# Performance work log

Hardware: AMD Instinct MI355X
Metric: run time of the kernel (lower is better)

The kernel has to match this reference:

```python
import jax, jax.numpy as jnp
import numpy as np

# irreps layout: in/out = 32x0e + 8x1o  (dim 32 + 24 = 56), sh = 1x0e + 1x1o (dim 4)
NS, NV = 32, 8
N_NODES, N_EDGES, N_EDGE_FEAT, HIDDEN = 10000, 100000, 64, 64
W_NUMEL = NS*NS + NS*NV + NV*NV + NV*NS  # 1600
EPS = 1e-5
# path normalization (e3nn-style 'component'/'element'):
# fan_in into 0e output = 32 (0x0 path) + 8 (1x1 path) = 40; same for 1o output.
INV40 = 1.0 / np.sqrt(40.0)            # paths with trivial/identity CG net factor
INV120 = 1.0 / np.sqrt(120.0)          # paths with w3j = delta/sqrt(3) extra factor


def setup_inputs() -> dict:
    key = jax.random.key(0)
    ks = jax.random.split(key, 12)
    node_attr = jax.random.normal(ks[0], (N_NODES, 56), dtype=jnp.float32)
    edge_attr = jax.random.normal(ks[1], (N_EDGES, N_EDGE_FEAT), dtype=jnp.float32)
    edge_sh = jax.random.normal(ks[2], (N_EDGES, 4), dtype=jnp.float32)
    edge_index = jax.random.randint(ks[3], (2, N_EDGES), 0, N_NODES, dtype=jnp.int64)
    s1 = 1.0 / np.sqrt(N_EDGE_FEAT)
    s2 = 1.0 / np.sqrt(HIDDEN)
    fc1_w = jax.random.normal(ks[4], (N_EDGE_FEAT, HIDDEN), dtype=jnp.float32) * s1
    fc1_b = jnp.zeros((HIDDEN,), dtype=jnp.float32)
    fc2_w = jax.random.normal(ks[5], (HIDDEN, W_NUMEL), dtype=jnp.float32) * s2
    fc2_b = jnp.zeros((W_NUMEL,), dtype=jnp.float32)
    bn_gamma0 = jnp.ones((NS,), dtype=jnp.float32)
    bn_beta0 = jnp.zeros((NS,), dtype=jnp.float32)
    bn_gamma1 = jnp.ones((NV,), dtype=jnp.float32)
    return dict(node_attr=node_attr, edge_attr=edge_attr, edge_sh=edge_sh,
                edge_index=edge_index, fc1_w=fc1_w, fc1_b=fc1_b,
                fc2_w=fc2_w, fc2_b=fc2_b, bn_gamma0=bn_gamma0,
                bn_beta0=bn_beta0, bn_gamma1=bn_gamma1)


def _forward(node_attr, edge_attr, edge_sh, fc1_w, fc1_b, fc2_w, fc2_b,
             bn_gamma0, bn_beta0, bn_gamma1, edge_index):
    E = edge_attr.shape[0]
    N = node_attr.shape[0]
    edge_src, edge_dst = edge_index[0], edge_index[1]

    # edge MLP -> per-edge tensor-product weights [E, 1600]
    h = jax.nn.relu(edge_attr @ fc1_w + fc1_b)
    w = h @ fc2_w + fc2_b
    o1 = NS * NS            # 0e x 0e -> 0e
    o2 = o1 + NS * NV       # 0e x 1o -> 1o
    o3 = o2 + NV * NV       # 1o x 0e -> 1o
    w00 = w[:, :o1].reshape(E, NS, NS)
    w01 = w[:, o1:o2].reshape(E, NS, NV)
    w10 = w[:, o2:o3].reshape(E, NV, NV)
    w11 = w[:, o3:].reshape(E, NV, NS)

    # gather node features at destination, split into scalar / vector irreps
    x = node_attr[edge_dst]                  # [E, 56]
    x0 = x[:, :NS]                           # [E, 32] scalars
    x1 = x[:, NS:].reshape(E, NV, 3)         # [E, 8, 3] l=1 vectors
    s0 = edge_sh[:, 0]                       # [E]
    s1 = edge_sh[:, 1:4]                     # [E, 3]

    # Clebsch-Gordan paths (w3j(1,1,0)=w3j(1,0,1)=w3j(0,1,1)=delta/sqrt(3))
    out0 = jnp.einsum('eu,euw->ew', x0 * s0[:, None], w00) * INV40 \
         + jnp.einsum('eui,ei,euw->ew', x1, s1, w11) * INV120
    out1 = jnp.einsum('eu,ei,euw->ewi', x0, s1, w01) * INV40 \
         + jnp.einsum('eui,euw->ewi', x1 * s0[:, None, None], w10) * INV40
    tp_out = jnp.concatenate([out0, out1.reshape(E, NV * 3)], axis=-1)  # [E, 56]

    # scatter-mean over edge_src
    sums = jax.ops.segment_sum(tp_out, edge_src, num_segments=N)
    cnt = jax.ops.segment_sum(jnp.ones((E,), tp_out.dtype), edge_src, num_segments=N)
    out = sums / jnp.maximum(cnt, 1.0)[:, None]

    # residual (in_dim == out_dim, pad is a no-op)
    out = out + node_attr

    # e3nn-style BatchNorm (training statistics, reduce='mean')
    sc = out[:, :NS]
    vec = out[:, NS:].reshape(N, NV, 3)
    m = sc.mean(axis=0)
    sc_c = sc - m
    var = (sc_c ** 2).mean(axis=0)
    sc_n = sc_c * jax.lax.rsqrt(var + EPS) * bn_gamma0 + bn_beta0
    vnorm = (vec ** 2).mean(axis=-1).mean(axis=0)          # [NV]
    vec_n = vec * (jax.lax.rsqrt(vnorm + EPS) * bn_gamma1)[None, :, None]
    return jnp.concatenate([sc_n, vec_n.reshape(N, NV * 3)], axis=-1)


def reference(node_attr, edge_attr, edge_sh, edge_index, fc1_w, fc1_b,
              fc2_w, fc2_b, bn_gamma0, bn_beta0, bn_gamma1):
    return _forward(node_attr, edge_attr, edge_sh, fc1_w, fc1_b, fc2_w,
                    fc2_b, bn_gamma0, bn_beta0, bn_gamma1, edge_index)
```

## Files before the change

### kernel.cpp

```cpp
#include <hip/hip_runtime.h>

typedef __attribute__((ext_vector_type(4))) float f32x4;
typedef __attribute__((ext_vector_type(2))) float f32x2;
typedef __attribute__((ext_vector_type(8))) short bf16x8;

#define NEDGE 100000
#define NNODE 10000
#define INV40f 0.15811388300841897f
#define INV120f 0.09128709291752769f

__device__ inline short f2bf(float f) {
    unsigned u = __builtin_bit_cast(unsigned, f);
    u = (u + 0x7fffu + ((u >> 16) & 1u)) >> 16;
    return (short)u;
}

__device__ __forceinline__ float bperm(int byteIdx, float v) {
    return __builtin_bit_cast(float,
        __builtin_amdgcn_ds_bpermute(byteIdx, __builtin_bit_cast(int, v)));
}

__device__ __forceinline__ void stage16(const void* gsrc, void* ldst) {
    __builtin_amdgcn_global_load_lds(
        (const __attribute__((address_space(1))) unsigned*)gsrc,
        (__attribute__((address_space(3))) unsigned*)(unsigned long long)(uintptr_t)ldst,
        16, 0, 0);
}

#define MFMA16(A,B,C) __builtin_amdgcn_mfma_f32_16x16x32_bf16((A),(B),(C),0,0,0)

__global__ __launch_bounds__(256) void prep(const float* __restrict__ fc1_w,
                                            const float* __restrict__ fc2_w,
                                            short* __restrict__ fc1_wt,
                                            short* __restrict__ fc2_wt,
                                            float* __restrict__ stats,
                                            int* __restrict__ hist) {
    const int b = blockIdx.x, t = threadIdx.x;
    if (b < 25) {
        __shared__ short tile[64 * 66];
        const int c0 = b * 64;
        #pragma unroll
        for (int rep = 0; rep < 16; rep++) {
            const int idx = rep * 256 + t;
            const int k = idx >> 6, c = idx & 63;
            tile[k * 66 + c] = f2bf(fc2_w[(size_t)k * 1600 + c0 + c]);
        }
        __syncthreads();
        #pragma unroll
        for (int rep = 0; rep < 16; rep++) {
            const int idx = rep * 256 + t;
            const int c = idx >> 6, k = idx & 63;
            fc2_wt[(size_t)(c0 + c) * 64 + k] = tile[k * 66 + c];
        }
    } else if (b == 25) {
        #pragma unroll
        for (int rep = 0; rep < 16; rep++) {
            const int i = rep * 256 + t;
            fc1_wt[(i & 63) * 64 + (i >> 6)] = f2bf(fc1_w[i]);
        }
    } else if (b == 26) {
        if (t < 72) stats[t] = 0.0f;
    } else {
        const int i = (b - 27) * 256 + t;
        if (i < NNODE) hist[i] = 0;
    }
}

__global__ __launch_bounds__(512, 4) void edge_fused(
    const float* __restrict__ node_attr,
    const float* __restrict__ edge_attr,
    const float* __restrict__ edge_sh,
    const int*   __restrict__ edge_index,
    const float* __restrict__ fc1_b,
    const float* __restrict__ fc2_b,
    const short* __restrict__ fc1_wt,
    const short* __restrict__ fc2_wt,
    float* __restrict__ tp_out,
    int*   __restrict__ hist)
{
    __shared__ __align__(16) char lds[51200];
    char* cbA = lds;
    char* cbB = lds + 16384;

    const int tid  = threadIdx.x;
    const int wid  = tid >> 6;
    const int wtid = tid & 63;
    const int l15  = wtid & 15;
    const int lg   = wtid >> 4;
    const int lg4  = lg * 4;
    const int e0   = blockIdx.x * 128 + wid * 16;
    const bool active = (e0 < NEDGE);

    char*  h_s = lds + 32768 + wid * 2048;
    float* shb = (float*)(lds + 49152 + wid * 256);

#define STAGE1(CH, BUF, J) do { \
        const int _o = (wid * 2 + (J)) * 1024 + wtid * 16; \
        const int _g = _o ^ (((_o >> 7) & 7) << 4); \
        stage16((const char*)fc2_wt + (CH) * 16384 + _g, (BUF) + (wid * 2 + (J)) * 1024); \
    } while (0)
#define STAGE_FULL(CH, BUF) do { STAGE1(CH, BUF, 0); STAGE1(CH, BUF, 1); } while (0)
#define STAGE_TAIL(CH, BUF) do { if (wid < 4) { STAGE1(CH, BUF, 0); STAGE1(CH, BUF, 1); } } while (0)

    STAGE_FULL(0, cbA);

    int dst_r = 0;
    if (active && wtid < 16) {
        dst_r = edge_index[NEDGE + e0 + wtid];
        const int src = edge_index[e0 + wtid];
        const f32x4 sh_r = *(const f32x4*)(edge_sh + (size_t)(e0 + wtid) * 4);
        atomicAdd(&hist[src], 1);
        *(f32x4*)(shb + wtid * 4) = sh_r;
    }

    bf16x8 ha0, ha1;
    f32x4 shv = {0.f, 0.f, 0.f, 0.f};
    float c00r[8], cb1r[8], c10r[6], c11r[2];
    int vidx[4];
    #pragma unroll
    for (int g = 0; g < 4; g++) vidx[g] = (g * 16 + l15) * 4;

    if (active) {
        const float* pa = edge_attr + (size_t)(e0 + l15) * 64 + lg * 8;
        const f32x4 va0 = *(const f32x4*)(pa);
        const f32x4 va1 = *(const f32x4*)(pa + 4);
        const f32x4 va2 = *(const f32x4*)(pa + 32);
        const f32x4 va3 = *(const f32x4*)(pa + 36);

        const int dstm = __shfl(dst_r, l15, 64);
        const float* nap = node_attr + (size_t)dstm * 56;
        const f32x4 x0a = *(const f32x4*)(nap + lg * 8);
        const f32x4 x0b = *(const f32x4*)(nap + lg * 8 + 4);
        const f32x2 x1a = *(const f32x2*)(nap + 32 + lg * 6);
        const f32x2 x1b = *(const f32x2*)(nap + 34 + lg * 6);
        const f32x2 x1c = *(const f32x2*)(nap + 36 + lg * 6);
        shv = *(const f32x4*)(shb + l15 * 4);

        const float s0 = shv[0];
        #pragma unroll
        for (int j = 0; j < 4; j++) {
            cb1r[j]     = INV40f * x0a[j];
            cb1r[4 + j] = INV40f * x0b[j];
            c00r[j]     = s0 * cb1r[j];
            c00r[4 + j] = s0 * cb1r[4 + j];
        }
        const float i40s0 = INV40f * s0;
        c10r[0] = i40s0 * x1a[0]; c10r[1] = i40s0 * x1a[1]; c10r[2] = i40s0 * x1b[0];
        c10r[3] = i40s0 * x1b[1]; c10r[4] = i40s0 * x1c[0]; c10r[5] = i40s0 * x1c[1];
        c11r[0] = INV120f * (x1a[0]*shv[1] + x1a[1]*shv[2] + x1b[0]*shv[3]);
        c11r[1] = INV120f * (x1b[1]*shv[1] + x1c[0]*shv[2] + x1c[1]*shv[3]);

        bf16x8 a0, a1;
        #pragma unroll
        for (int i = 0; i < 4; i++) {
            a0[i] = f2bf(va0[i]); a0[4+i] = f2bf(va1[i]);
            a1[i] = f2bf(va2[i]); a1[4+i] = f2bf(va3[i]);
        }
        #pragma unroll
        for (int nf0 = 0; nf0 < 4; nf0++) {
            const bf16x8 b0 = *(const bf16x8*)(fc1_wt + (nf0*16 + l15)*64 + lg*8);
            const bf16x8 b1 = *(const bf16x8*)(fc1_wt + (nf0*16 + l15)*64 + 32 + lg*8);
            const float bias = fc1_b[nf0*16 + l15];
            f32x4 c = {bias, bias, bias, bias};
            c = MFMA16(a0, b0, c);
            c = MFMA16(a1, b1, c);
            #pragma unroll
            for (int reg = 0; reg < 4; reg++) {
                const int row = lg4 + reg;
                *(short*)(h_s + ((row*128 + (nf0*16 + l15)*2) ^ ((row & 7) << 4))) =
                    f2bf(fmaxf(c[reg], 0.0f));
            }
        }
        ha0 = *(const bf16x8*)(h_s + ((l15*128 +      lg*16) ^ ((l15 & 7) << 4)));
        ha1 = *(const bf16x8*)(h_s + ((l15*128 + 64 + lg*16) ^ ((l15 & 7) << 4)));
    }

    const int s_swz = (l15 & 7) << 4;
    const int ro0 = (l15 * 128 + lg * 16) ^ s_swz;
    const int ro1 = (l15 * 128 + lg * 16 + 64) ^ s_swz;
    const int usel = lg >> 1;
    float acc0[2][4] = {{0,0,0,0},{0,0,0,0}};
    float ab1[4] = {0,0,0,0};
    float b2v[12] = {};

    auto frag = [&](const char* cb, int nfl, int nf) -> f32x4 {
        const bf16x8 b0 = *(const bf16x8*)(cb + nfl * 2048 + ro0);
        const bf16x8 b1 = *(const bf16x8*)(cb + nfl * 2048 + ro1);
        f32x4 c = *(const f32x4*)(fc2_b + nf * 16 + lg4);
        c = MFMA16(b0, ha0, c);
        return MFMA16(b1, ha1, c);
    };
    auto cons_w00 = [&](const char* cb, int ch) {
        #pragma unroll
        for (int nfl = 0; nfl < 8; nfl++) {
            const int nf = ch * 8 + nfl;
            const f32x4 c = frag(cb, nfl, nf);
            const int u = nf >> 1, hi = nf & 1;
            const float cv = bperm(vidx[u >> 3], c00r[u & 7]);
            #pragma unroll
            for (int reg = 0; reg < 4; reg++) acc0[hi][reg] += cv * c[reg];
        }
    };
    auto cons_w01 = [&](const char* cb, int rbase) {
        #pragma unroll
        for (int i = 0; i < 8; i++) {
            const int nfl_r = rbase + i;
            const f32x4 c = frag(cb, i, 64 + nfl_r);
            const int r0 = (2 * nfl_r) & 7, g = nfl_r >> 2;
            const float e0v = bperm(vidx[g], cb1r[r0]);
            const float e1v = bperm(vidx[g], cb1r[r0 + 1]);
            const float cv = usel ? e1v : e0v;
            #pragma unroll
            for (int reg = 0; reg < 4; reg++) ab1[reg] += cv * c[reg];
        }
    };
    auto cons_w10 = [&](const char* cb, int fb) {
        #pragma unroll
        for (int nfl = 0; nfl < 4; nfl++) {
            const f32x4 c = frag(cb, fb + nfl, 80 + nfl);
            #pragma unroll
            for (int i = 0; i < 3; i++) {
                const float e0v = bperm(vidx[nfl], c10r[i]);
                const float e1v = bperm(vidx[nfl], c10r[3 + i]);
                const float cv = usel ? e1v : e0v;
                #pragma unroll
                for (int reg = 0; reg < 4; reg++) b2v[reg * 3 + i] += cv * c[reg];
            }
        }
    };
    auto cons_w11 = [&](const char* cb, int fb, int ridx0, int cnt) {
        #pragma unroll
        for (int i = 0; i < 8; i++) {
            if (i >= cnt) break;
            const int ridx = ridx0 + i;
            const f32x4 c = frag(cb, fb + i, 84 + ridx);
            const int up = ridx >> 1, hi = ridx & 1;
            const float cv = bperm(vidx[up >> 1], c11r[up & 1]);
            #pragma unroll
            for (int reg = 0; reg < 4; reg++) acc0[hi][reg] += cv * c[reg];
        }
    };

    __syncthreads();
    STAGE_FULL(1,  cbB); if (active) cons_w00(cbA, 0); __syncthreads();
    STAGE_FULL(2,  cbA); if (active) cons_w00(cbB, 1); __syncthreads();
    STAGE_FULL(3,  cbB); if (active) cons_w00(cbA, 2); __syncthreads();
    STAGE_FULL(4,  cbA); if (active) cons_w00(cbB, 3); __syncthreads();
    STAGE_FULL(5,  cbB); if (active) cons_w00(cbA, 4); __syncthreads();
    STAGE_FULL(6,  cbA); if (active) cons_w00(cbB, 5); __syncthreads();
    STAGE_FULL(7,  cbB); if (active) cons_w00(cbA, 6); __syncthreads();
    STAGE_FULL(8,  cbA); if (active) cons_w00(cbB, 7); __syncthreads();
    STAGE_FULL(9,  cbB); if (active) cons_w01(cbA, 0); __syncthreads();
    STAGE_FULL(10, cbA); if (active) cons_w01(cbB, 8); __syncthreads();
    STAGE_FULL(11, cbB); if (active) { cons_w10(cbA, 0); cons_w11(cbA, 4, 0, 4); } __syncthreads();
    STAGE_TAIL(12, cbA); if (active) cons_w11(cbB, 0, 4, 8);   __syncthreads();
                         if (active) cons_w11(cbA, 0, 12, 4);

    if (!active) return;

    float* orow = tp_out + (size_t)(e0 + l15) * 56;
    {
        const f32x4 o0 = {acc0[0][0], acc0[0][1], acc0[0][2], acc0[0][3]};
        const f32x4 o1 = {acc0[1][0], acc0[1][1], acc0[1][2], acc0[1][3]};
        *(f32x4*)(orow + lg4)      = o0;
        *(f32x4*)(orow + 16 + lg4) = o1;
    }
    #pragma unroll
    for (int reg = 0; reg < 4; reg++) ab1[reg] += __shfl_xor(ab1[reg], 32, 64);
    #pragma unroll
    for (int m = 0; m < 12; m++) b2v[m] += __shfl_xor(b2v[m], 32, 64);
    if (lg < 2) {
        float ov[12];
        #pragma unroll
        for (int reg = 0; reg < 4; reg++) {
            ov[reg*3 + 0] = shv[1] * ab1[reg] + b2v[reg*3 + 0];
            ov[reg*3 + 1] = shv[2] * ab1[reg] + b2v[reg*3 + 1];
            ov[reg*3 + 2] = shv[3] * ab1[reg] + b2v[reg*3 + 2];
        }
        float* p1 = orow + 32 + lg * 12;
        *(f32x4*)(p1)     = f32x4{ov[0], ov[1], ov[2],  ov[3]};
        *(f32x4*)(p1 + 4) = f32x4{ov[4], ov[5], ov[6],  ov[7]};
        *(f32x4*)(p1 + 8) = f32x4{ov[8], ov[9], ov[10], ov[11]};
    }
#undef STAGE1
#undef STAGE_FULL
#undef STAGE_TAIL
}

__global__ __launch_bounds__(1024) void scan_hist(const int* __restrict__ hist,
                                                  int* __restrict__ offsets,
                                                  int* __restrict__ cursor) {
    __shared__ int part[1024];
    const int t = threadIdx.x;
    const int n0 = t * 10;
    int lh[10];
    int s = 0;
    if (n0 < NNODE) {
        #pragma unroll
        for (int j = 0; j < 10; j++) { lh[j] = hist[n0 + j]; s += lh[j]; }
    }
    part[t] = s;
    __syncthreads();
    for (int d = 1; d < 1024; d <<= 1) {
        const int v = (t >= d) ? part[t - d] : 0;
        __syncthreads();
        part[t] += v;
        __syncthreads();
    }
    if (n0 < NNODE) {
        int run = part[t] - s;
        #pragma unroll
        for (int j = 0; j < 10; j++) {
            offsets[n0 + j] = run; cursor[n0 + j] = run; run += lh[j];
        }
    }
    if (t == 0) offsets[NNODE] = NEDGE;
}

__global__ __launch_bounds__(256) void fill_perm(const int* __restrict__ edge_index,
                                                 int* __restrict__ cursor,
                                                 int* __restrict__ perm) {
    const int e = blockIdx.x * 256 + threadIdx.x;
    if (e < NEDGE) {
        const int s = edge_index[e];
        const int p = atomicAdd(&cursor[s], 1);
        perm[p] = e;
    }
}

__global__ __launch_bounds__(256) void node_agg(
    const float* __restrict__ tp_out, const int* __restrict__ offsets,
    const int* __restrict__ perm,
    const float* __restrict__ node_attr, float* __restrict__ out,
    float* __restrict__ stats)
{
    __shared__ float part[72];
    const int tid = threadIdx.x;
    if (tid < 72) part[tid] = 0.0f;
    __syncthreads();
    const int n = blockIdx.x * 16 + (tid >> 4);
    const int q = tid & 15;
    if (n < NNODE && q < 14) {
        const int st = offsets[n], en = offsets[n + 1];
        f32x4 acc = {0.f, 0.f, 0.f, 0.f};
        for (int r = st; r < en; r++)
            acc += *(const f32x4*)(tp_out + (size_t)perm[r] * 56 + q * 4);
        const float inv = 1.0f / fmaxf((float)(en - st), 1.0f);
        const int c0 = q * 4;
        const f32x4 res = *(const f32x4*)(node_attr + (size_t)n * 56 + c0);
        f32x4 val;
        #pragma unroll
        for (int j = 0; j < 4; j++) {
            val[j] = acc[j] * inv + res[j];
            const int c = c0 + j;
            if (c < 32) {
                atomicAdd(&part[c], val[j]);
                atomicAdd(&part[32 + c], val[j] * val[j]);
            } else {
                atomicAdd(&part[64 + (c - 32) / 3], val[j] * val[j]);
            }
        }
        *(f32x4*)(out + (size_t)n * 56 + c0) = val;
    }
    __syncthreads();
    if (tid < 72) unsafeAtomicAdd(&stats[tid], part[tid]);
}

__global__ __launch_bounds__(256) void node_norm(
    float* __restrict__ out, const float* __restrict__ stats,
    const float* __restrict__ g0, const float* __restrict__ b0,
    const float* __restrict__ g1)
{
    const int id = blockIdx.x * 256 + threadIdx.x;
    if (id >= NNODE * 56) return;
    const int c = id % 56;
    float val = out[id];
    if (c < 32) {
        const float m   = stats[c]      * (1.0f / NNODE);
        const float ex2 = stats[32 + c] * (1.0f / NNODE);
        const float var = ex2 - m * m;
        val = (val - m) * rsqrtf(var + 1e-5f) * g0[c] + b0[c];
    } else {
        const int v = (c - 32) / 3;
        const float vn = stats[64 + v] * (1.0f / (3.0f * NNODE));
        val = val * rsqrtf(vn + 1e-5f) * g1[v];
    }
    out[id] = val;
}

extern "C" void kernel_launch(void* const* d_in, const int* in_sizes, int n_in,
                              void* d_out, int out_size, void* d_ws, size_t ws_size,
                              hipStream_t stream) {
    const float* node_attr = (const float*)d_in[0];
    const float* edge_attr = (const float*)d_in[1];
    const float* edge_sh   = (const float*)d_in[2];
    const int*   edge_index= (const int*)  d_in[3];
    const float* fc1_w     = (const float*)d_in[4];
    const float* fc1_b     = (const float*)d_in[5];
    const float* fc2_w     = (const float*)d_in[6];
    const float* fc2_b     = (const float*)d_in[7];
    const float* g0        = (const float*)d_in[8];
    const float* b0        = (const float*)d_in[9];
    const float* g1        = (const float*)d_in[10];
    float* out = (float*)d_out;

    char* ws = (char*)d_ws;
    float* stats   = (float*)(ws + 0);
    int*   hist    = (int*)  (ws + 288);
    int*   offsets = (int*)  (ws + 40288);
    int*   cursor  = (int*)  (ws + 80320);
    int*   perm    = (int*)  (ws + 120320);
    short* fc1_wt  = (short*)(ws + 520320);
    short* fc2_wt  = (short*)(ws + 528512);
    float* tp_out  = (float*)(ws + 733312);

    prep<<<67, 256, 0, stream>>>(fc1_w, fc2_w, fc1_wt, fc2_wt, stats, hist);
    edge_fused<<<782, 512, 0, stream>>>(node_attr, edge_attr, edge_sh, edge_index,
                                        fc1_b, fc2_b, fc1_wt, fc2_wt, tp_out, hist);
    scan_hist<<<1, 1024, 0, stream>>>(hist, offsets, cursor);
    fill_perm<<<391, 256, 0, stream>>>(edge_index, cursor, perm);
    node_agg<<<625, 256, 0, stream>>>(tp_out, offsets, perm, node_attr, out, stats);
    node_norm<<<2188, 256, 0, stream>>>(out, stats, g0, b0, g1);
}
```

Measured before the change: 110.8 us.

## Prefetch fc2 fragments in registers, stage bias in LDS, use wave-shuffle scan

The fc2 consumer loops now keep a rolling 2-3 deep software pipeline of LDS B-fragment loads and bias loads in registers, so LDS latency overlaps the MFMAs. The fc2 bias is staged once per block into shared memory instead of being read from global memory for every fragment. The single-block histogram scan is rewritten as a 256-thread wave-shuffle scan with 40 nodes per thread, replacing the 1024-thread LDS scan and its many barriers. The tail stage now loads a full chunk. This raises LDS use and register pressure, which could lower occupancy.

```diff
diff --git a/kernel.cpp b/kernel.cpp
--- a/kernel.cpp
+++ b/kernel.cpp
@@ -78,9 +78,10 @@
     float* __restrict__ tp_out,
     int*   __restrict__ hist)
 {
-    __shared__ __align__(16) char lds[51200];
+    __shared__ __align__(16) char lds[57600];
     char* cbA = lds;
     char* cbB = lds + 16384;
+    float* bias_s = (float*)(lds + 51200);
 
     const int tid  = threadIdx.x;
     const int wid  = tid >> 6;
@@ -100,9 +101,12 @@
         stage16((const char*)fc2_wt + (CH) * 16384 + _g, (BUF) + (wid * 2 + (J)) * 1024); \
     } while (0)
 #define STAGE_FULL(CH, BUF) do { STAGE1(CH, BUF, 0); STAGE1(CH, BUF, 1); } while (0)
-#define STAGE_TAIL(CH, BUF) do { if (wid < 4) { STAGE1(CH, BUF, 0); STAGE1(CH, BUF, 1); } } while (0)
 
     STAGE_FULL(0, cbA);
+
+    if (tid < 400) {
+        *(f32x4*)(bias_s + tid * 4) = *(const f32x4*)(fc2_b + tid * 4);
+    }
 
     int dst_r = 0;
     if (active && wtid < 16) {
@@ -175,26 +179,35 @@
         ha1 = *(const bf16x8*)(h_s + ((l15*128 + 64 + lg*16) ^ ((l15 & 7) << 4)));
     }
 
-    const int s_swz = (l15 & 7) << 4;
-    const int ro0 = (l15 * 128 + lg * 16) ^ s_swz;
-    const int ro1 = (l15 * 128 + lg * 16 + 64) ^ s_swz;
+    const int hswz = (l15 & 7) << 4;
+    const int ro0 = (l15 * 128 + lg * 16) ^ hswz;
+    const int ro1 = (l15 * 128 + lg * 16 + 64) ^ hswz;
     const int usel = lg >> 1;
     float acc0[2][4] = {{0,0,0,0},{0,0,0,0}};
     float ab1[4] = {0,0,0,0};
     float b2v[12] = {};
 
-    auto frag = [&](const char* cb, int nfl, int nf) -> f32x4 {
-        const bf16x8 b0 = *(const bf16x8*)(cb + nfl * 2048 + ro0);
-        const bf16x8 b1 = *(const bf16x8*)(cb + nfl * 2048 + ro1);
-        f32x4 c = *(const f32x4*)(fc2_b + nf * 16 + lg4);
-        c = MFMA16(b0, ha0, c);
-        return MFMA16(b1, ha1, c);
-    };
     auto cons_w00 = [&](const char* cb, int ch) {
-        #pragma unroll
-        for (int nfl = 0; nfl < 8; nfl++) {
-            const int nf = ch * 8 + nfl;
-            const f32x4 c = frag(cb, nfl, nf);
+        bf16x8 pb0[3], pb1[3]; f32x4 pc[3];
+        #pragma unroll
+        for (int k = 0; k < 3; k++) {
+            pb0[k] = *(const bf16x8*)(cb + k * 2048 + ro0);
+            pb1[k] = *(const bf16x8*)(cb + k * 2048 + ro1);
+            pc[k]  = *(const f32x4*)(bias_s + (ch * 8 + k) * 16 + lg4);
+        }
+        #pragma unroll
+        for (int i = 0; i < 8; i++) {
+            const int s = i % 3;
+            const bf16x8 b0 = pb0[s], b1 = pb1[s];
+            f32x4 c = pc[s];
+            if (i + 3 < 8) {
+                pb0[s] = *(const bf16x8*)(cb + (i + 3) * 2048 + ro0);
+                pb1[s] = *(const bf16x8*)(cb + (i + 3) * 2048 + ro1);
+                pc[s]  = *(const f32x4*)(bias_s + (ch * 8 + i + 3) * 16 + lg4);
+            }
+            c = MFMA16(b0, ha0, c);
+            c = MFMA16(b1, ha1, c);
+            const int nf = ch * 8 + i;
             const int u = nf >> 1, hi = nf & 1;
             const float cv = bperm(vidx[u >> 3], c00r[u & 7]);
             #pragma unroll
@@ -202,10 +215,26 @@
         }
     };
     auto cons_w01 = [&](const char* cb, int rbase) {
+        bf16x8 pb0[3], pb1[3]; f32x4 pc[3];
+        #pragma unroll
+        for (int k = 0; k < 3; k++) {
+            pb0[k] = *(const bf16x8*)(cb + k * 2048 + ro0);
+            pb1[k] = *(const bf16x8*)(cb + k * 2048 + ro1);
+            pc[k]  = *(const f32x4*)(bias_s + (64 + rbase + k) * 16 + lg4);
+        }
         #pragma unroll
         for (int i = 0; i < 8; i++) {
+            const int s = i % 3;
+            const bf16x8 b0 = pb0[s], b1 = pb1[s];
+            f32x4 c = pc[s];
+            if (i + 3 < 8) {
+                pb0[s] = *(const bf16x8*)(cb + (i + 3) * 2048 + ro0);
+                pb1[s] = *(const bf16x8*)(cb + (i + 3) * 2048 + ro1);
+                pc[s]  = *(const f32x4*)(bias_s + (64 + rbase + i + 3) * 16 + lg4);
+            }
+            c = MFMA16(b0, ha0, c);
+            c = MFMA16(b1, ha1, c);
             const int nfl_r = rbase + i;
-            const f32x4 c = frag(cb, i, 64 + nfl_r);
             const int r0 = (2 * nfl_r) & 7, g = nfl_r >> 2;
             const float e0v = bperm(vidx[g], cb1r[r0]);
             const float e1v = bperm(vidx[g], cb1r[r0 + 1]);
@@ -215,25 +244,83 @@
         }
     };
     auto cons_w10 = [&](const char* cb, int fb) {
-        #pragma unroll
-        for (int nfl = 0; nfl < 4; nfl++) {
-            const f32x4 c = frag(cb, fb + nfl, 80 + nfl);
+        bf16x8 pb0[2], pb1[2]; f32x4 pc[2];
+        #pragma unroll
+        for (int k = 0; k < 2; k++) {
+            pb0[k] = *(const bf16x8*)(cb + (fb + k) * 2048 + ro0);
+            pb1[k] = *(const bf16x8*)(cb + (fb + k) * 2048 + ro1);
+            pc[k]  = *(const f32x4*)(bias_s + (80 + k) * 16 + lg4);
+        }
+        #pragma unroll
+        for (int i = 0; i < 4; i++) {
+            const int s = i % 2;
+            const bf16x8 b0 = pb0[s], b1 = pb1[s];
+            f32x4 c = pc[s];
+            if (i + 2 < 4) {
+                pb0[s] = *(const bf16x8*)(cb + (fb + i + 2) * 2048 + ro0);
+                pb1[s] = *(const bf16x8*)(cb + (fb + i + 2) * 2048 + ro1);
+                pc[s]  = *(const f32x4*)(bias_s + (80 + i + 2) * 16 + lg4);
+            }
+            c = MFMA16(b0, ha0, c);
+            c = MFMA16(b1, ha1, c);
             #pragma unroll
-            for (int i = 0; i < 3; i++) {
-                const float e0v = bperm(vidx[nfl], c10r[i]);
-                const float e1v = bperm(vidx[nfl], c10r[3 + i]);
+            for (int k = 0; k < 3; k++) {
+                const float e0v = bperm(vidx[i], c10r[k]);
+                const float e1v = bperm(vidx[i], c10r[3 + k]);
                 const float cv = usel ? e1v : e0v;
                 #pragma unroll
-                for (int reg = 0; reg < 4; reg++) b2v[reg * 3 + i] += cv * c[reg];
+                for (int reg = 0; reg < 4; reg++) b2v[reg * 3 + k] += cv * c[reg];
             }
         }
     };
-    auto cons_w11 = [&](const char* cb, int fb, int ridx0, int cnt) {
+    auto cons_w11_4 = [&](const char* cb, int fb, int ridx0) {
+        bf16x8 pb0[2], pb1[2]; f32x4 pc[2];
+        #pragma unroll
+        for (int k = 0; k < 2; k++) {
+            pb0[k] = *(const bf16x8*)(cb + (fb + k) * 2048 + ro0);
+            pb1[k] = *(const bf16x8*)(cb + (fb + k) * 2048 + ro1);
+            pc[k]  = *(const f32x4*)(bias_s + (84 + ridx0 + k) * 16 + lg4);
+        }
+        #pragma unroll
+        for (int i = 0; i < 4; i++) {
+            const int s = i % 2;
+            const bf16x8 b0 = pb0[s], b1 = pb1[s];
+            f32x4 c = pc[s];
+            if (i + 2 < 4) {
+                pb0[s] = *(const bf16x8*)(cb + (fb + i + 2) * 2048 + ro0);
+                pb1[s] = *(const bf16x8*)(cb + (fb + i + 2) * 2048 + ro1);
+                pc[s]  = *(const f32x4*)(bias_s + (84 + ridx0 + i + 2) * 16 + lg4);
+            }
+            c = MFMA16(b0, ha0, c);
+            c = MFMA16(b1, ha1, c);
+            const int ridx = ridx0 + i;
+            const int up = ridx >> 1, hi = ridx & 1;
+            const float cv = bperm(vidx[up >> 1], c11r[up & 1]);
+            #pragma unroll
+            for (int reg = 0; reg < 4; reg++) acc0[hi][reg] += cv * c[reg];
+        }
+    };
+    auto cons_w11_8 = [&](const char* cb, int ridx0) {
+        bf16x8 pb0[3], pb1[3]; f32x4 pc[3];
+        #pragma unroll
+        for (int k = 0; k < 3; k++) {
+            pb0[k] = *(const bf16x8*)(cb + k * 2048 + ro0);
+            pb1[k] = *(const bf16x8*)(cb + k * 2048 + ro1);
+            pc[k]  = *(const f32x4*)(bias_s + (84 + ridx0 + k) * 16 + lg4);
+        }
         #pragma unroll
         for (int i = 0; i < 8; i++) {
-            if (i >= cnt) break;
+            const int s = i % 3;
+            const bf16x8 b0 = pb0[s], b1 = pb1[s];
+            f32x4 c = pc[s];
+            if (i + 3 < 8) {
+                pb0[s] = *(const bf16x8*)(cb + (i + 3) * 2048 + ro0);
+                pb1[s] = *(const bf16x8*)(cb + (i + 3) * 2048 + ro1);
+                pc[s]  = *(const f32x4*)(bias_s + (84 + ridx0 + i + 3) * 16 + lg4);
+            }
+            c = MFMA16(b0, ha0, c);
+            c = MFMA16(b1, ha1, c);
             const int ridx = ridx0 + i;
-            const f32x4 c = frag(cb, fb + i, 84 + ridx);
             const int up = ridx >> 1, hi = ridx & 1;
             const float cv = bperm(vidx[up >> 1], c11r[up & 1]);
             #pragma unroll
@@ -252,9 +339,9 @@
     STAGE_FULL(8,  cbA); if (active) cons_w00(cbB, 7); __syncthreads();
     STAGE_FULL(9,  cbB); if (active) cons_w01(cbA, 0); __syncthreads();
     STAGE_FULL(10, cbA); if (active) cons_w01(cbB, 8); __syncthreads();
-    STAGE_FULL(11, cbB); if (active) { cons_w10(cbA, 0); cons_w11(cbA, 4, 0, 4); } __syncthreads();
-    STAGE_TAIL(12, cbA); if (active) cons_w11(cbB, 0, 4, 8);   __syncthreads();
-                         if (active) cons_w11(cbA, 0, 12, 4);
+    STAGE_FULL(11, cbB); if (active) { cons_w10(cbA, 0); cons_w11_4(cbA, 4, 0); } __syncthreads();
+    STAGE_FULL(12, cbA); if (active) cons_w11_8(cbB, 4); __syncthreads();
+                         if (active) cons_w11_4(cbA, 0, 12);
 
     if (!active) return;
 
@@ -284,34 +371,35 @@
     }
 #undef STAGE1
 #undef STAGE_FULL
-#undef STAGE_TAIL
-}
-
-__global__ __launch_bounds__(1024) void scan_hist(const int* __restrict__ hist,
-                                                  int* __restrict__ offsets,
-                                                  int* __restrict__ cursor) {
-    __shared__ int part[1024];
+}
+
+__global__ __launch_bounds__(256) void scan_hist(const int* __restrict__ hist,
+                                                 int* __restrict__ offsets,
+                                                 int* __restrict__ cursor) {
+    __shared__ int wsum[4];
     const int t = threadIdx.x;
-    const int n0 = t * 10;
-    int lh[10];
+    const int lane = t & 63;
+    const int w = t >> 6;
+    const int n0 = t * 40;
     int s = 0;
     if (n0 < NNODE) {
-        #pragma unroll
-        for (int j = 0; j < 10; j++) { lh[j] = hist[n0 + j]; s += lh[j]; }
-    }
-    part[t] = s;
+        for (int j = 0; j < 40; j++) s += hist[n0 + j];
+    }
+    int incl = s;
+    #pragma unroll
+    for (int d = 1; d < 64; d <<= 1) {
+        const int v = __shfl_up(incl, d, 64);
+        if (lane >= d) incl += v;
+    }
+    if (lane == 63) wsum[w] = incl;
     __syncthreads();
-    for (int d = 1; d < 1024; d <<= 1) {
-        const int v = (t >= d) ? part[t - d] : 0;
-        __syncthreads();
-        part[t] += v;
-        __syncthreads();
-    }
+    int base = 0;
+    for (int ww = 0; ww < 4; ww++) base += (ww < w) ? wsum[ww] : 0;
     if (n0 < NNODE) {
-        int run = part[t] - s;
-        #pragma unroll
-        for (int j = 0; j < 10; j++) {
-            offsets[n0 + j] = run; cursor[n0 + j] = run; run += lh[j];
+        int run = base + incl - s;
+        for (int j = 0; j < 40; j++) {
+            const int h = hist[n0 + j];
+            offsets[n0 + j] = run; cursor[n0 + j] = run; run += h;
         }
     }
     if (t == 0) offsets[NNODE] = NEDGE;
@@ -417,7 +505,7 @@
     prep<<<67, 256, 0, stream>>>(fc1_w, fc2_w, fc1_wt, fc2_wt, stats, hist);
     edge_fused<<<782, 512, 0, stream>>>(node_attr, edge_attr, edge_sh, edge_index,
                                         fc1_b, fc2_b, fc1_wt, fc2_wt, tp_out, hist);
-    scan_hist<<<1, 1024, 0, stream>>>(hist, offsets, cursor);
+    scan_hist<<<1, 256, 0, stream>>>(hist, offsets, cursor);
     fill_perm<<<391, 256, 0, stream>>>(edge_index, cursor, perm);
     node_agg<<<625, 256, 0, stream>>>(tp_out, offsets, perm, node_attr, out, stats);
     node_norm<<<2188, 256, 0, stream>>>(out, stats, g0, b0, g1);
```

Measured after the change: 103.7 us. 6.3% less time.

## Switch edge kernel to 32x32x16 MFMA with 32 edges per wave

Applied to the files above, without the earlier changes.

The fused edge kernel moves from 16x16x32 to 32x32x16 bf16 MFMA tiles. Each wave now handles 32 edges, blocks shrink to 4 waves, fc2 bias is cached in LDS, and the hidden activations reuse the second staging buffer. This is meant to halve B-fragment LDS reads per edge and remove the cross-half shuffles in the epilogue, at the cost of more accumulator registers and lower occupancy. The histogram scan is also rewritten as a 256-thread wave-shuffle scan instead of a 1024-thread LDS Hillis-Steele loop.

```diff
diff --git a/kernel.cpp b/kernel.cpp
--- a/kernel.cpp
+++ b/kernel.cpp
@@ -1,8 +1,9 @@
 #include <hip/hip_runtime.h>
 
-typedef __attribute__((ext_vector_type(4))) float f32x4;
-typedef __attribute__((ext_vector_type(2))) float f32x2;
-typedef __attribute__((ext_vector_type(8))) short bf16x8;
+typedef __attribute__((ext_vector_type(4)))  float f32x4;
+typedef __attribute__((ext_vector_type(16))) float f32x16;
+typedef __attribute__((ext_vector_type(8)))  short bf16x8;
+typedef __attribute__((ext_vector_type(4)))  short short4v;
 
 #define NEDGE 100000
 #define NNODE 10000
@@ -27,7 +28,7 @@
         16, 0, 0);
 }
 
-#define MFMA16(A,B,C) __builtin_amdgcn_mfma_f32_16x16x32_bf16((A),(B),(C),0,0,0)
+#define MFMA32(A,B,C) __builtin_amdgcn_mfma_f32_32x32x16_bf16((A),(B),(C),0,0,0)
 
 __global__ __launch_bounds__(256) void prep(const float* __restrict__ fc1_w,
                                             const float* __restrict__ fc2_w,
@@ -66,7 +67,7 @@
     }
 }
 
-__global__ __launch_bounds__(512, 4) void edge_fused(
+__global__ __launch_bounds__(256, 2) void edge_fused(
     const float* __restrict__ node_attr,
     const float* __restrict__ edge_attr,
     const float* __restrict__ edge_sh,
@@ -78,166 +79,192 @@
     float* __restrict__ tp_out,
     int*   __restrict__ hist)
 {
-    __shared__ __align__(16) char lds[51200];
+    __shared__ __align__(16) char lds[41216];
     char* cbA = lds;
     char* cbB = lds + 16384;
+    float* bias_s = (float*)(lds + 34816);
 
     const int tid  = threadIdx.x;
     const int wid  = tid >> 6;
     const int wtid = tid & 63;
-    const int l15  = wtid & 15;
-    const int lg   = wtid >> 4;
-    const int lg4  = lg * 4;
-    const int e0   = blockIdx.x * 128 + wid * 16;
+    const int l31  = wtid & 31;
+    const int half = wtid >> 5;
+    const int e0   = blockIdx.x * 128 + wid * 32;
     const bool active = (e0 < NEDGE);
 
-    char*  h_s = lds + 32768 + wid * 2048;
-    float* shb = (float*)(lds + 49152 + wid * 256);
+    char*  h_s = cbB + wid * 4096;
+    float* shb = (float*)(lds + 32768 + wid * 512);
+    const int swzl = (l31 & 7) << 4;
 
 #define STAGE1(CH, BUF, J) do { \
-        const int _o = (wid * 2 + (J)) * 1024 + wtid * 16; \
+        const int _o = (wid * 4 + (J)) * 1024 + wtid * 16; \
         const int _g = _o ^ (((_o >> 7) & 7) << 4); \
-        stage16((const char*)fc2_wt + (CH) * 16384 + _g, (BUF) + (wid * 2 + (J)) * 1024); \
+        stage16((const char*)fc2_wt + (CH) * 16384 + _g, (BUF) + (wid * 4 + (J)) * 1024); \
     } while (0)
-#define STAGE_FULL(CH, BUF) do { STAGE1(CH, BUF, 0); STAGE1(CH, BUF, 1); } while (0)
-#define STAGE_TAIL(CH, BUF) do { if (wid < 4) { STAGE1(CH, BUF, 0); STAGE1(CH, BUF, 1); } } while (0)
+#define STAGE_FULL(CH, BUF) do { STAGE1(CH,BUF,0); STAGE1(CH,BUF,1); STAGE1(CH,BUF,2); STAGE1(CH,BUF,3); } while (0)
 
     STAGE_FULL(0, cbA);
 
+    *(f32x4*)(bias_s + tid * 4) = *(const f32x4*)(fc2_b + tid * 4);
+    if (tid < 144)
+        *(f32x4*)(bias_s + (tid + 256) * 4) = *(const f32x4*)(fc2_b + (tid + 256) * 4);
+
     int dst_r = 0;
-    if (active && wtid < 16) {
+    if (active && wtid < 32) {
         dst_r = edge_index[NEDGE + e0 + wtid];
-        const int src = edge_index[e0 + wtid];
-        const f32x4 sh_r = *(const f32x4*)(edge_sh + (size_t)(e0 + wtid) * 4);
-        atomicAdd(&hist[src], 1);
-        *(f32x4*)(shb + wtid * 4) = sh_r;
-    }
-
-    bf16x8 ha0, ha1;
+        atomicAdd(&hist[edge_index[e0 + wtid]], 1);
+        *(f32x4*)(shb + wtid * 4) = *(const f32x4*)(edge_sh + (size_t)(e0 + wtid) * 4);
+    }
+
+    bf16x8 hb[4];
     f32x4 shv = {0.f, 0.f, 0.f, 0.f};
-    float c00r[8], cb1r[8], c10r[6], c11r[2];
-    int vidx[4];
-    #pragma unroll
-    for (int g = 0; g < 4; g++) vidx[g] = (g * 16 + l15) * 4;
+    float cb1r[16], c10r[12], c11r[4];
+    int vs[2];
+    vs[0] = l31 * 4;
+    vs[1] = (32 + l31) * 4;
 
     if (active) {
-        const float* pa = edge_attr + (size_t)(e0 + l15) * 64 + lg * 8;
-        const f32x4 va0 = *(const f32x4*)(pa);
-        const f32x4 va1 = *(const f32x4*)(pa + 4);
-        const f32x4 va2 = *(const f32x4*)(pa + 32);
-        const f32x4 va3 = *(const f32x4*)(pa + 36);
-
-        const int dstm = __shfl(dst_r, l15, 64);
+        const int dstm = __shfl(dst_r, l31, 64);
         const float* nap = node_attr + (size_t)dstm * 56;
-        const f32x4 x0a = *(const f32x4*)(nap + lg * 8);
-        const f32x4 x0b = *(const f32x4*)(nap + lg * 8 + 4);
-        const f32x2 x1a = *(const f32x2*)(nap + 32 + lg * 6);
-        const f32x2 x1b = *(const f32x2*)(nap + 34 + lg * 6);
-        const f32x2 x1c = *(const f32x2*)(nap + 36 + lg * 6);
-        shv = *(const f32x4*)(shb + l15 * 4);
-
-        const float s0 = shv[0];
+        shv = *(const f32x4*)(shb + l31 * 4);
+
+        const f32x4 t0 = *(const f32x4*)(nap + half * 16);
+        const f32x4 t1 = *(const f32x4*)(nap + half * 16 + 4);
+        const f32x4 t2 = *(const f32x4*)(nap + half * 16 + 8);
+        const f32x4 t3 = *(const f32x4*)(nap + half * 16 + 12);
         #pragma unroll
         for (int j = 0; j < 4; j++) {
-            cb1r[j]     = INV40f * x0a[j];
-            cb1r[4 + j] = INV40f * x0b[j];
-            c00r[j]     = s0 * cb1r[j];
-            c00r[4 + j] = s0 * cb1r[4 + j];
-        }
-        const float i40s0 = INV40f * s0;
-        c10r[0] = i40s0 * x1a[0]; c10r[1] = i40s0 * x1a[1]; c10r[2] = i40s0 * x1b[0];
-        c10r[3] = i40s0 * x1b[1]; c10r[4] = i40s0 * x1c[0]; c10r[5] = i40s0 * x1c[1];
-        c11r[0] = INV120f * (x1a[0]*shv[1] + x1a[1]*shv[2] + x1b[0]*shv[3]);
-        c11r[1] = INV120f * (x1b[1]*shv[1] + x1c[0]*shv[2] + x1c[1]*shv[3]);
-
-        bf16x8 a0, a1;
-        #pragma unroll
-        for (int i = 0; i < 4; i++) {
-            a0[i] = f2bf(va0[i]); a0[4+i] = f2bf(va1[i]);
-            a1[i] = f2bf(va2[i]); a1[4+i] = f2bf(va3[i]);
-        }
-        #pragma unroll
-        for (int nf0 = 0; nf0 < 4; nf0++) {
-            const bf16x8 b0 = *(const bf16x8*)(fc1_wt + (nf0*16 + l15)*64 + lg*8);
-            const bf16x8 b1 = *(const bf16x8*)(fc1_wt + (nf0*16 + l15)*64 + 32 + lg*8);
-            const float bias = fc1_b[nf0*16 + l15];
-            f32x4 c = {bias, bias, bias, bias};
-            c = MFMA16(a0, b0, c);
-            c = MFMA16(a1, b1, c);
-            #pragma unroll
-            for (int reg = 0; reg < 4; reg++) {
-                const int row = lg4 + reg;
-                *(short*)(h_s + ((row*128 + (nf0*16 + l15)*2) ^ ((row & 7) << 4))) =
-                    f2bf(fmaxf(c[reg], 0.0f));
-            }
-        }
-        ha0 = *(const bf16x8*)(h_s + ((l15*128 +      lg*16) ^ ((l15 & 7) << 4)));
-        ha1 = *(const bf16x8*)(h_s + ((l15*128 + 64 + lg*16) ^ ((l15 & 7) << 4)));
-    }
-
-    const int s_swz = (l15 & 7) << 4;
-    const int ro0 = (l15 * 128 + lg * 16) ^ s_swz;
-    const int ro1 = (l15 * 128 + lg * 16 + 64) ^ s_swz;
-    const int usel = lg >> 1;
-    float acc0[2][4] = {{0,0,0,0},{0,0,0,0}};
+            cb1r[j]      = INV40f * t0[j];
+            cb1r[4 + j]  = INV40f * t1[j];
+            cb1r[8 + j]  = INV40f * t2[j];
+            cb1r[12 + j] = INV40f * t3[j];
+        }
+        const f32x4 y0 = *(const f32x4*)(nap + 32 + half * 12);
+        const f32x4 y1 = *(const f32x4*)(nap + 32 + half * 12 + 4);
+        const f32x4 y2 = *(const f32x4*)(nap + 32 + half * 12 + 8);
+        float xx[12];
+        #pragma unroll
+        for (int j = 0; j < 4; j++) { xx[j] = y0[j]; xx[4 + j] = y1[j]; xx[8 + j] = y2[j]; }
+        const float i40s0 = INV40f * shv[0];
+        #pragma unroll
+        for (int k = 0; k < 12; k++) c10r[k] = i40s0 * xx[k];
+        #pragma unroll
+        for (int e = 0; e < 4; e++)
+            c11r[e] = INV120f * (xx[e*3]*shv[1] + xx[e*3+1]*shv[2] + xx[e*3+2]*shv[3]);
+
+        const float* pe = edge_attr + (size_t)(e0 + l31) * 64 + half * 8;
+        bf16x8 eb[4];
+        #pragma unroll
+        for (int s = 0; s < 4; s++) {
+            const f32x4 a = *(const f32x4*)(pe + s * 16);
+            const f32x4 b = *(const f32x4*)(pe + s * 16 + 4);
+            #pragma unroll
+            for (int i = 0; i < 4; i++) { eb[s][i] = f2bf(a[i]); eb[s][4 + i] = f2bf(b[i]); }
+        }
+        #pragma unroll
+        for (int g = 0; g < 2; g++) {
+            f32x16 c;
+            #pragma unroll
+            for (int q = 0; q < 4; q++) {
+                const f32x4 bq = *(const f32x4*)(fc1_b + g*32 + q*8 + half*4);
+                c[q*4+0] = bq[0]; c[q*4+1] = bq[1]; c[q*4+2] = bq[2]; c[q*4+3] = bq[3];
+            }
+            #pragma unroll
+            for (int s = 0; s < 4; s++) {
+                const bf16x8 af = *(const bf16x8*)(fc1_wt + (g*32 + l31)*64 + s*16 + half*8);
+                c = MFMA32(af, eb[s], c);
+            }
+            #pragma unroll
+            for (int q = 0; q < 4; q++) {
+                short4v p;
+                #pragma unroll
+                for (int j = 0; j < 4; j++) p[j] = f2bf(fmaxf(c[q*4+j], 0.0f));
+                *(short4v*)(h_s + (l31*128 + ((g*64 + q*16 + half*8) ^ swzl)));
+                *(short4v*)(h_s + (l31*128 + ((g*64 + q*16 + half*8) ^ swzl))) = p;
+            }
+        }
+        #pragma unroll
+        for (int s = 0; s < 4; s++)
+            hb[s] = *(const bf16x8*)(h_s + (l31*128 + ((s*32 + half*16) ^ swzl)));
+    }
+
+    float acc0[16] = {};
     float ab1[4] = {0,0,0,0};
-    float b2v[12] = {};
-
-    auto frag = [&](const char* cb, int nfl, int nf) -> f32x4 {
-        const bf16x8 b0 = *(const bf16x8*)(cb + nfl * 2048 + ro0);
-        const bf16x8 b1 = *(const bf16x8*)(cb + nfl * 2048 + ro1);
-        f32x4 c = *(const f32x4*)(fc2_b + nf * 16 + lg4);
-        c = MFMA16(b0, ha0, c);
-        return MFMA16(b1, ha1, c);
-    };
+    float b2[12] = {};
+
+    auto mload = [&](const char* cb, int go, int G) -> f32x16 {
+        f32x16 c;
+        #pragma unroll
+        for (int q = 0; q < 4; q++) {
+            const f32x4 bq = *(const f32x4*)(bias_s + G*32 + q*8 + half*4);
+            c[q*4+0] = bq[0]; c[q*4+1] = bq[1]; c[q*4+2] = bq[2]; c[q*4+3] = bq[3];
+        }
+        #pragma unroll
+        for (int s = 0; s < 4; s++) {
+            const bf16x8 a = *(const bf16x8*)(cb + go*4096 + l31*128 + ((s*32 + half*16) ^ swzl));
+            c = MFMA32(a, hb[s], c);
+        }
+        return c;
+    };
+
     auto cons_w00 = [&](const char* cb, int ch) {
         #pragma unroll
-        for (int nfl = 0; nfl < 8; nfl++) {
-            const int nf = ch * 8 + nfl;
-            const f32x4 c = frag(cb, nfl, nf);
-            const int u = nf >> 1, hi = nf & 1;
-            const float cv = bperm(vidx[u >> 3], c00r[u & 7]);
-            #pragma unroll
-            for (int reg = 0; reg < 4; reg++) acc0[hi][reg] += cv * c[reg];
-        }
-    };
-    auto cons_w01 = [&](const char* cb, int rbase) {
-        #pragma unroll
-        for (int i = 0; i < 8; i++) {
-            const int nfl_r = rbase + i;
-            const f32x4 c = frag(cb, i, 64 + nfl_r);
-            const int r0 = (2 * nfl_r) & 7, g = nfl_r >> 2;
-            const float e0v = bperm(vidx[g], cb1r[r0]);
-            const float e1v = bperm(vidx[g], cb1r[r0 + 1]);
-            const float cv = usel ? e1v : e0v;
-            #pragma unroll
-            for (int reg = 0; reg < 4; reg++) ab1[reg] += cv * c[reg];
-        }
-    };
-    auto cons_w10 = [&](const char* cb, int fb) {
-        #pragma unroll
-        for (int nfl = 0; nfl < 4; nfl++) {
-            const f32x4 c = frag(cb, fb + nfl, 80 + nfl);
-            #pragma unroll
-            for (int i = 0; i < 3; i++) {
-                const float e0v = bperm(vidx[nfl], c10r[i]);
-                const float e1v = bperm(vidx[nfl], c10r[3 + i]);
-                const float cv = usel ? e1v : e0v;
+        for (int go = 0; go < 4; go++) {
+            const int G = ch * 4 + go;
+            const f32x16 c = mload(cb, go, G);
+            const float cv = shv[0] * bperm(vs[G >> 4], cb1r[G & 15]);
+            #pragma unroll
+            for (int r = 0; r < 16; r++) acc0[r] += cv * c[r];
+        }
+    };
+    auto cons_w01 = [&](const char* cb, int Gl0) {
+        #pragma unroll
+        for (int go = 0; go < 4; go++) {
+            const int Gl = Gl0 + go;
+            const f32x16 c = mload(cb, go, 32 + Gl);
+            #pragma unroll
+            for (int q = 0; q < 4; q++) {
+                const int u = Gl * 4 + q;
+                const float cvq = bperm(vs[u >> 4], cb1r[u & 15]);
                 #pragma unroll
-                for (int reg = 0; reg < 4; reg++) b2v[reg * 3 + i] += cv * c[reg];
-            }
-        }
-    };
-    auto cons_w11 = [&](const char* cb, int fb, int ridx0, int cnt) {
-        #pragma unroll
-        for (int i = 0; i < 8; i++) {
-            if (i >= cnt) break;
-            const int ridx = ridx0 + i;
-            const f32x4 c = frag(cb, fb + i, 84 + ridx);
-            const int up = ridx >> 1, hi = ridx & 1;
-            const float cv = bperm(vidx[up >> 1], c11r[up & 1]);
-            #pragma unroll
-            for (int reg = 0; reg < 4; reg++) acc0[hi][reg] += cv * c[reg];
+                for (int j = 0; j < 4; j++) ab1[j] += cvq * c[q*4+j];
+            }
+        }
+    };
+    auto cons_w10 = [&](const char* cb) {
+        #pragma unroll
+        for (int go = 0; go < 2; go++) {
+            const f32x16 c = mload(cb, go, 40 + go);
+            #pragma unroll
+            for (int q = 0; q < 4; q++) {
+                const int u = go * 4 + q;
+                #pragma unroll
+                for (int i = 0; i < 3; i++) {
+                    const float cv = bperm(vs[u >> 2], c10r[(u & 3) * 3 + i]);
+                    #pragma unroll
+                    for (int j = 0; j < 4; j++) b2[j*3+i] += cv * c[q*4+j];
+                }
+            }
+        }
+    };
+    auto cons_w11_2 = [&](const char* cb, int goBase, int Gl0) {
+        #pragma unroll
+        for (int go = 0; go < 2; go++) {
+            const int Gl = Gl0 + go;
+            const f32x16 c = mload(cb, goBase + go, 42 + Gl);
+            const float cv = bperm(vs[Gl >> 2], c11r[Gl & 3]);
+            #pragma unroll
+            for (int r = 0; r < 16; r++) acc0[r] += cv * c[r];
+        }
+    };
+    auto cons_w11_4 = [&](const char* cb, int Gl0) {
+        #pragma unroll
+        for (int go = 0; go < 4; go++) {
+            const int Gl = Gl0 + go;
+            const f32x16 c = mload(cb, go, 42 + Gl);
+            const float cv = bperm(vs[Gl >> 2], c11r[Gl & 3]);
+            #pragma unroll
+            for (int r = 0; r < 16; r++) acc0[r] += cv * c[r];
         }
     };
 
@@ -251,67 +278,59 @@
     STAGE_FULL(7,  cbB); if (active) cons_w00(cbA, 6); __syncthreads();
     STAGE_FULL(8,  cbA); if (active) cons_w00(cbB, 7); __syncthreads();
     STAGE_FULL(9,  cbB); if (active) cons_w01(cbA, 0); __syncthreads();
-    STAGE_FULL(10, cbA); if (active) cons_w01(cbB, 8); __syncthreads();
-    STAGE_FULL(11, cbB); if (active) { cons_w10(cbA, 0); cons_w11(cbA, 4, 0, 4); } __syncthreads();
-    STAGE_TAIL(12, cbA); if (active) cons_w11(cbB, 0, 4, 8);   __syncthreads();
-                         if (active) cons_w11(cbA, 0, 12, 4);
+    STAGE_FULL(10, cbA); if (active) cons_w01(cbB, 4); __syncthreads();
+    STAGE_FULL(11, cbB); if (active) { cons_w10(cbA); cons_w11_2(cbA, 2, 0); } __syncthreads();
+    STAGE_FULL(12, cbA); if (active) cons_w11_4(cbB, 2); __syncthreads();
+                         if (active) cons_w11_2(cbA, 0, 6);
 
     if (!active) return;
 
-    float* orow = tp_out + (size_t)(e0 + l15) * 56;
-    {
-        const f32x4 o0 = {acc0[0][0], acc0[0][1], acc0[0][2], acc0[0][3]};
-        const f32x4 o1 = {acc0[1][0], acc0[1][1], acc0[1][2], acc0[1][3]};
-        *(f32x4*)(orow + lg4)      = o0;
-        *(f32x4*)(orow + 16 + lg4) = o1;
-    }
+    float* orow = tp_out + (size_t)(e0 + l31) * 56;
     #pragma unroll
-    for (int reg = 0; reg < 4; reg++) ab1[reg] += __shfl_xor(ab1[reg], 32, 64);
+    for (int q = 0; q < 4; q++)
+        *(f32x4*)(orow + q*8 + half*4) = f32x4{acc0[q*4], acc0[q*4+1], acc0[q*4+2], acc0[q*4+3]};
+    float ov[12];
     #pragma unroll
-    for (int m = 0; m < 12; m++) b2v[m] += __shfl_xor(b2v[m], 32, 64);
-    if (lg < 2) {
-        float ov[12];
-        #pragma unroll
-        for (int reg = 0; reg < 4; reg++) {
-            ov[reg*3 + 0] = shv[1] * ab1[reg] + b2v[reg*3 + 0];
-            ov[reg*3 + 1] = shv[2] * ab1[reg] + b2v[reg*3 + 1];
-            ov[reg*3 + 2] = shv[3] * ab1[reg] + b2v[reg*3 + 2];
-        }
-        float* p1 = orow + 32 + lg * 12;
-        *(f32x4*)(p1)     = f32x4{ov[0], ov[1], ov[2],  ov[3]};
-        *(f32x4*)(p1 + 4) = f32x4{ov[4], ov[5], ov[6],  ov[7]};
-        *(f32x4*)(p1 + 8) = f32x4{ov[8], ov[9], ov[10], ov[11]};
-    }
+    for (int j = 0; j < 4; j++) {
+        ov[j*3 + 0] = shv[1] * ab1[j] + b2[j*3 + 0];
+        ov[j*3 + 1] = shv[2] * ab1[j] + b2[j*3 + 1];
+        ov[j*3 + 2] = shv[3] * ab1[j] + b2[j*3 + 2];
+    }
+    float* p1 = orow + 32 + half * 12;
+    *(f32x4*)(p1)     = f32x4{ov[0], ov[1], ov[2],  ov[3]};
+    *(f32x4*)(p1 + 4) = f32x4{ov[4], ov[5], ov[6],  ov[7]};
+    *(f32x4*)(p1 + 8) = f32x4{ov[8], ov[9], ov[10], ov[11]};
 #undef STAGE1
 #undef STAGE_FULL
-#undef STAGE_TAIL
-}
-
-__global__ __launch_bounds__(1024) void scan_hist(const int* __restrict__ hist,
-                                                  int* __restrict__ offsets,
-                                                  int* __restrict__ cursor) {
-    __shared__ int part[1024];
+}
+
+__global__ __launch_bounds__(256) void scan_hist(const int* __restrict__ hist,
+                                                 int* __restrict__ offsets,
+                                                 int* __restrict__ cursor) {
+    __shared__ int wsum[4];
     const int t = threadIdx.x;
-    const int n0 = t * 10;
-    int lh[10];
+    const int lane = t & 63;
+    const int w = t >> 6;
+    const int n0 = t * 40;
     int s = 0;
     if (n0 < NNODE) {
-        #pragma unroll
-        for (int j = 0; j < 10; j++) { lh[j] = hist[n0 + j]; s += lh[j]; }
-    }
-    part[t] = s;
+        for (int j = 0; j < 40; j++) s += hist[n0 + j];
+    }
+    int incl = s;
+    #pragma unroll
+    for (int d = 1; d < 64; d <<= 1) {
+        const int v = __shfl_up(incl, d, 64);
+        if (lane >= d) incl += v;
+    }
+    if (lane == 63) wsum[w] = incl;
     __syncthreads();
-    for (int d = 1; d < 1024; d <<= 1) {
-        const int v = (t >= d) ? part[t - d] : 0;
-        __syncthreads();
-        part[t] += v;
-        __syncthreads();
-    }
+    int base = 0;
+    for (int ww = 0; ww < 4; ww++) base += (ww < w) ? wsum[ww] : 0;
     if (n0 < NNODE) {
-        int run = part[t] - s;
-        #pragma unroll
-        for (int j = 0; j < 10; j++) {
-            offsets[n0 + j] = run; cursor[n0 + j] = run; run += lh[j];
+        int run = base + incl - s;
+        for (int j = 0; j < 40; j++) {
+            const int h = hist[n0 + j];
+            offsets[n0 + j] = run; cursor[n0 + j] = run; run += h;
         }
     }
     if (t == 0) offsets[NNODE] = NEDGE;
@@ -415,9 +434,9 @@
     float* tp_out  = (float*)(ws + 733312);
 
     prep<<<67, 256, 0, stream>>>(fc1_w, fc2_w, fc1_wt, fc2_wt, stats, hist);
-    edge_fused<<<782, 512, 0, stream>>>(node_attr, edge_attr, edge_sh, edge_index,
+    edge_fused<<<782, 256, 0, stream>>>(node_attr, edge_attr, edge_sh, edge_index,
                                         fc1_b, fc2_b, fc1_wt, fc2_wt, tp_out, hist);
-    scan_hist<<<1, 1024, 0, stream>>>(hist, offsets, cursor);
+    scan_hist<<<1, 256, 0, stream>>>(hist, offsets, cursor);
     fill_perm<<<391, 256, 0, stream>>>(edge_index, cursor, perm);
     node_agg<<<625, 256, 0, stream>>>(tp_out, offsets, perm, node_attr, out, stats);
     node_norm<<<2188, 256, 0, stream>>>(out, stats, g0, b0, g1);
```

Measured after the change: 105.0 us. 5.2% less time.
